# Performance work log

Measured on AMD Instinct MI355X. Metric: run time of the kernel, lower is better.

## Reference

```python
import jax, jax.numpy as jnp
import numpy as np

# Module constants (match init_kwargs)
E = 8           # num_experts
K = 2           # num_experts_per_tok
BLOCK = 16      # BLOCK_SIZE hardcoded in module
NORM_TOPK = True


def setup_inputs() -> dict:
    key = jax.random.key(0)
    k0, k1, k2, k3 = jax.random.split(key, 4)
    B, S, H = 2, 2048, 768
    F = 4 * H  # ffn_hidden_size
    x = jax.random.normal(k0, (B, S, H), dtype=jnp.float32)
    router_w = jax.random.normal(k1, (E, H), dtype=jnp.float32) * 0.02
    # kaiming-uniform-ish scale for w1/w2
    w1 = jax.random.uniform(k2, (H, E * F), dtype=jnp.float32, minval=-1.0, maxval=1.0) * float(1.0 / np.sqrt(H))
    w2 = jax.random.uniform(k3, (E * F, H), dtype=jnp.float32, minval=-1.0, maxval=1.0) * float(1.0 / np.sqrt(E * F))
    return {"x": x, "router_w": router_w, "w1": w1, "w2": w2}


def _moe_forward(x, router_w, w1, w2):
    B, S, H = x.shape
    T = B * S
    x_flat = x.reshape(T, H)

    # Router
    router_logits = x_flat @ router_w.T                      # [T, E]
    rw = jax.nn.softmax(router_logits.astype(jnp.float32), axis=-1)
    top_w, sel = jax.lax.top_k(rw, K)                        # [T, K]
    if NORM_TOPK:
        top_w = top_w / top_w.sum(axis=-1, keepdims=True)
    top_w = top_w.astype(x.dtype)  # NOTE: computed but NOT applied in combine (faithful to source)

    # Block-padding multiplicities (faithful to source's duplicate-last-token padding bug):
    # assignments are sorted stably by expert; the LAST assignment of each expert's
    # group is duplicated pad_e = (-count_e) % BLOCK times and then scatter-added.
    sel_flat = sel.reshape(-1)                               # [T*K], token-major stable order
    flat_idx = jnp.arange(T * K, dtype=jnp.int32)
    counts = jax.ops.segment_sum(jnp.ones((T * K,), jnp.int32), sel_flat, num_segments=E)
    pad = (-counts) % BLOCK                                  # [E]
    last_idx = jax.ops.segment_max(flat_idx, sel_flat, num_segments=E)  # [E]
    mult = 1 + jnp.where(flat_idx == last_idx[sel_flat], pad[sel_flat], 0)  # [T*K]

    # Combine coefficients coef[t, e] = multiplicity of (token t, expert e) assignment
    token_ids = flat_idx // K
    coef = jnp.zeros((T, E), dtype=x.dtype).at[token_ids, sel_flat].add(mult.astype(x.dtype))

    # Expert FFNs: y1 = gelu(x @ W1_e) @ W2_e, combined with coef (NOT routing weights)
    F = w1.shape[1] // E
    w1e = w1.reshape(H, E, F)
    w2e = w2.reshape(E, F, H)
    out = jnp.zeros((T, H), dtype=x.dtype)
    for e in range(E):  # small fixed loop over experts
        h = jax.nn.gelu(x_flat @ w1e[:, e, :], approximate=False)  # [T, F]
        out = out + coef[:, e:e + 1] * (h @ w2e[e])                # [T, H]

    return out.reshape(B, S, H), router_logits


def reference(x, router_w, w1, w2):
    return _moe_forward(x, router_w, w1, w2)
```

## Files before the change

kernel.cpp:

```cpp
#include <hip/hip_runtime.h>
#include <math.h>

#define T_TOK 4096
#define H_DIM 768
#define E_NUM 8
#define F_DIM 3072
#define EF_DIM 24576
#define BK 64
#define SEG_MAX 9216
#define MAX_TILES 72

#define OFF_CNT      0
#define OFF_LAST     8
#define OFF_NT      40
#define OFF_TOTAL   41
#define OFF_SCHED_E 48
#define OFF_SCHED_G 120

#define WS_SEL   768
#define WS_TOK   33536
#define WS_COEF  70400
#define WS_XG    107264ull
#define WS_HG    14263040ull
#define WS_WT    70886144ull

typedef __attribute__((ext_vector_type(8))) short short8;
typedef __attribute__((ext_vector_type(4))) float float4v;

__device__ __forceinline__ short f2b(float f) {
  union { float f; unsigned u; } v; v.f = f;
  unsigned r = v.u + 0x7FFFu + ((v.u >> 16) & 1u);
  return (short)(r >> 16);
}
__device__ __forceinline__ float gelu_fast(float v) {
  const float z = 1.5957691216f * fmaf(0.044715f * v * v, v, v);
  return v / (1.0f + __expf(-z));
}
__device__ __forceinline__ void gl_lds16(const void* g, void* l) {
  __builtin_amdgcn_global_load_lds(
      (const __attribute__((address_space(1))) void*)g,
      (__attribute__((address_space(3))) void*)l, 16, 0, 0);
}

__global__ __launch_bounds__(256) void router_k(const float* __restrict__ x,
                                                const float* __restrict__ rw,
                                                float* __restrict__ logits_out,
                                                int* __restrict__ sel) {
  __shared__ float rws[E_NUM * H_DIM];
  for (int i = threadIdx.x; i < E_NUM * H_DIM; i += 256) rws[i] = rw[i];
  __syncthreads();
  const int wid = threadIdx.x >> 6, lane = threadIdx.x & 63;
  const int t = blockIdx.x * 4 + wid;
  const float* xr = x + (size_t)t * H_DIM;
  double acc[E_NUM];
#pragma unroll
  for (int e = 0; e < E_NUM; ++e) acc[e] = 0.0;
  for (int i = 0; i < H_DIM / 64; ++i) {
    const int h = lane + 64 * i;
    const float xv = xr[h];
#pragma unroll
    for (int e = 0; e < E_NUM; ++e) acc[e] += (double)xv * (double)rws[e * H_DIM + h];
  }
#pragma unroll
  for (int e = 0; e < E_NUM; ++e)
    for (int off = 32; off; off >>= 1) acc[e] += __shfl_down(acc[e], off);
  if (lane == 0) {
    float lg[E_NUM];
#pragma unroll
    for (int e = 0; e < E_NUM; ++e) { lg[e] = (float)acc[e]; logits_out[t * E_NUM + e] = lg[e]; }
    int e0 = 0;
    for (int e = 1; e < E_NUM; ++e) if (lg[e] > lg[e0]) e0 = e;
    int e1 = -1;
    for (int e = 0; e < E_NUM; ++e) {
      if (e == e0) continue;
      if (e1 < 0 || lg[e] > lg[e1]) e1 = e;
    }
    sel[t * 2 + 0] = e0;
    sel[t * 2 + 1] = e1;
  }
}

__global__ __launch_bounds__(1024) void hist_k(const int* __restrict__ sel,
                                               int* __restrict__ meta) {
  const int e = blockIdx.x;
  const int tid = threadIdx.x, lane = tid & 63, wid = tid >> 6;
  __shared__ int wcnt[16], wlast[16];
  int c = 0, lmax = 0;
#pragma unroll
  for (int it = 0; it < 8; ++it) {
    const int a = it * 1024 + tid;
    const unsigned long long mask = __ballot(sel[a] == e);
    if (lane == 0 && mask) {
      c += (int)__popcll(mask);
      const int hi = 63 - (int)__clzll((long long)mask);
      const int cand = a + hi + 1;
      lmax = lmax > cand ? lmax : cand;
    }
  }
  if (lane == 0) { wcnt[wid] = c; wlast[wid] = lmax; }
  __syncthreads();
  if (tid == 0) {
    int C = 0, L = 0;
    for (int w = 0; w < 16; ++w) { C += wcnt[w]; L = L > wlast[w] ? L : wlast[w]; }
    meta[OFF_CNT + e] = C;
    meta[OFF_LAST + e] = L;
  }
}

__global__ __launch_bounds__(1024) void scatter_k(const int* __restrict__ sel,
                                                  int* __restrict__ meta,
                                                  int* __restrict__ tok,
                                                  float* __restrict__ coefv) {
  const int e = blockIdx.x;
  const int tid = threadIdx.x, lane = tid & 63, wid = tid >> 6;
  __shared__ int wv[16];

  int cnt[E_NUM];
#pragma unroll
  for (int i = 0; i < E_NUM; ++i) cnt[i] = meta[OFF_CNT + i];
  int seg = 0;
  for (int i = 0; i < e; ++i) seg += (cnt[i] + 127) & ~127;
  const int c = cnt[e];
  const int ru = (c + 127) & ~127;
  const int pad = (16 - (c & 15)) & 15;
  const int laste = meta[OFF_LAST + e];
  const float lastcoef = (float)(1 + pad);

  for (int p = c + tid; p < ru; p += 1024) { tok[seg + p] = -1; coefv[seg + p] = 0.0f; }
  if (e == E_NUM - 1) {
    const int total = seg + ru;
    for (int p = total + tid; p < SEG_MAX; p += 1024) { tok[p] = -1; coefv[p] = 0.0f; }
  }

  if (e == 0) {
    int nt = 0, s2 = 0;
    for (int i = 0; i < E_NUM; ++i) {
      const int rui = (cnt[i] + 127) & ~127;
      for (int m = 0; m < rui; m += 128) {
        if (nt == tid) { meta[OFF_SCHED_E + nt] = i; meta[OFF_SCHED_G + nt] = s2 + m; }
        ++nt;
      }
      s2 += rui;
    }
    if (tid >= nt && tid < MAX_TILES) { meta[OFF_SCHED_E + tid] = -1; meta[OFF_SCHED_G + tid] = 0; }
    if (tid == 0) { meta[OFF_NT] = nt; meta[OFF_TOTAL] = s2; }
  }

  int running = 0;
#pragma unroll
  for (int it = 0; it < 8; ++it) {
    const int a = it * 1024 + tid;
    const bool f = (sel[a] == e);
    const unsigned long long mask = __ballot(f);
    if (lane == 0) wv[wid] = (int)__popcll(mask);
    __syncthreads();
    int pre = 0, tot = 0;
#pragma unroll
    for (int w = 0; w < 16; ++w) { const int v = wv[w]; pre += (w < wid) ? v : 0; tot += v; }
    if (f) {
      const int rank = (int)__popcll(mask & ((1ull << lane) - 1ull));
      const int g = seg + running + pre + rank;
      tok[g] = a >> 1;
      coefv[g] = (laste == a + 1) ? lastcoef : 1.0f;
    }
    running += tot;
    __syncthreads();
  }
}

__global__ __launch_bounds__(256) void gather_x_k(const float* __restrict__ x,
                                                  const int* __restrict__ tok,
                                                  short* __restrict__ xg) {
  const int u = blockIdx.x * 256 + threadIdx.x;
  const int g = u / 96;
  const int c = (u - g * 96) * 8;
  const int t = tok[g];
  short8 v = {0, 0, 0, 0, 0, 0, 0, 0};
  if (t >= 0) {
    const float* src = x + (size_t)t * H_DIM + c;
    float4v f0 = *(const float4v*)src;
    float4v f1 = *(const float4v*)(src + 4);
    v[0] = f2b(f0[0]); v[1] = f2b(f0[1]); v[2] = f2b(f0[2]); v[3] = f2b(f0[3]);
    v[4] = f2b(f1[0]); v[5] = f2b(f1[1]); v[6] = f2b(f1[2]); v[7] = f2b(f1[3]);
  }
  *(short8*)&xg[(size_t)g * H_DIM + c] = v;
}

__global__ __launch_bounds__(256) void conv_w1_k(const float* __restrict__ w1, short* __restrict__ w1t) {
  __shared__ float tile[64][65];
  const int n0 = blockIdx.x * 64;
  const int h0 = blockIdx.y * 64;
  const int tid = threadIdx.x;
  const int rr = tid >> 4;
  const int cc = (tid & 15) * 4;
#pragma unroll
  for (int p = 0; p < 4; ++p) {
    const int r = p * 16 + rr;
    float4v f = *(const float4v*)(w1 + (size_t)(h0 + r) * EF_DIM + n0 + cc);
    tile[r][cc] = f[0]; tile[r][cc + 1] = f[1]; tile[r][cc + 2] = f[2]; tile[r][cc + 3] = f[3];
  }
  __syncthreads();
#pragma unroll
  for (int p = 0; p < 2; ++p) {
    const int item = p * 256 + tid;
    const int nl = item >> 3;
    const int u8 = (item & 7) * 8;
    short8 v;
#pragma unroll
    for (int j = 0; j < 8; ++j) v[j] = f2b(tile[u8 + j][nl]);
    *(short8*)(w1t + (size_t)(n0 + nl) * H_DIM + h0 + u8) = v;
  }
}

__global__ __launch_bounds__(256) void conv_w2_k(const float* __restrict__ w2, short* __restrict__ w2t) {
  __shared__ float tile[64][65];
  const int k0 = blockIdx.x * 64;
  const int h0 = blockIdx.y * 64;
  const int e = k0 / F_DIM;
  const int f0 = k0 - e * F_DIM;
  const int tid = threadIdx.x;
  const int rr = tid >> 4;
  const int cc = (tid & 15) * 4;
#pragma unroll
  for (int p = 0; p < 4; ++p) {
    const int r = p * 16 + rr;
    float4v f = *(const float4v*)(w2 + (size_t)(k0 + r) * H_DIM + h0 + cc);
    tile[r][cc] = f[0]; tile[r][cc + 1] = f[1]; tile[r][cc + 2] = f[2]; tile[r][cc + 3] = f[3];
  }
  __syncthreads();
#pragma unroll
  for (int p = 0; p < 2; ++p) {
    const int item = p * 256 + tid;
    const int nl = item >> 3;
    const int u8 = (item & 7) * 8;
    short8 v;
#pragma unroll
    for (int j = 0; j < 8; ++j) v[j] = f2b(tile[u8 + j][nl]);
    *(short8*)(w2t + (size_t)(e * H_DIM + h0 + nl) * F_DIM + f0 + u8) = v;
  }
}


__global__ __launch_bounds__(256) void gemm1_k(const short* __restrict__ xg,
                                               const short* __restrict__ w1t,
                                               const int* __restrict__ meta,
                                               short* __restrict__ hg) {
  const unsigned hwL = blockIdx.x;
  const unsigned logical = (hwL & 7u) * 216u + (hwL >> 3);
  const int slot = (int)(logical / 24u);
  const int n0 = (int)(logical % 24u) * 128;
  if (slot >= meta[OFF_NT]) return;
  const int e = meta[OFF_SCHED_E + slot];
  const int gbase = meta[OFF_SCHED_G + slot];

  __shared__ short As[128 * BK];
  __shared__ short Bs[128 * BK];

  const int tid = threadIdx.x;
  const int w = tid >> 6, l = tid & 63;
  const int mw = (w & 1) * 64, nw = (w >> 1) * 64;
  const int lrow = l & 15, q = l >> 4;

  const int srow = l >> 3;
  const int schunk = (l & 7) ^ srow;
  const short* agp[4];
  const short* bgp[4];
  short* alp[4];
  short* blp[4];
#pragma unroll
  for (int i = 0; i < 4; ++i) {
    const int r = i * 32 + w * 8 + srow;
    agp[i] = xg + (size_t)(gbase + r) * H_DIM + schunk * 8;
    bgp[i] = w1t + (size_t)(e * F_DIM + n0 + r) * H_DIM + schunk * 8;
    alp[i] = &As[(i * 32 + w * 8) * BK + l * 8];
    blp[i] = &Bs[(i * 32 + w * 8) * BK + l * 8];
  }
  const int rsw = lrow & 7;

  float4v acc[4][4] = {};

  for (int k0 = 0; k0 < H_DIM; k0 += BK) {
#pragma unroll
    for (int i = 0; i < 4; ++i) gl_lds16(agp[i] + k0, alp[i]);
#pragma unroll
    for (int i = 0; i < 4; ++i) gl_lds16(bgp[i] + k0, blp[i]);
    __syncthreads();
#pragma unroll
    for (int s = 0; s < 2; ++s) {
      short8 a_frag[4], b_frag[4];
      const int csw = ((s * 4 + q) ^ rsw) * 8;
#pragma unroll
      for (int i = 0; i < 4; ++i) a_frag[i] = *(const short8*)&As[(mw + 16 * i + lrow) * BK + csw];
#pragma unroll
      for (int j = 0; j < 4; ++j) b_frag[j] = *(const short8*)&Bs[(nw + 16 * j + lrow) * BK + csw];
#pragma unroll
      for (int i = 0; i < 4; ++i)
#pragma unroll
        for (int j = 0; j < 4; ++j)
          acc[i][j] = __builtin_amdgcn_mfma_f32_16x16x32_bf16(a_frag[i], b_frag[j], acc[i][j], 0, 0, 0);
    }
    __syncthreads();
  }
#pragma unroll
  for (int i = 0; i < 4; ++i)
#pragma unroll
    for (int j = 0; j < 4; ++j)
#pragma unroll
      for (int r = 0; r < 4; ++r) {
        const int row = mw + 16 * i + q * 4 + r;
        const int col = nw + 16 * j + lrow;
        hg[(size_t)(gbase + row) * F_DIM + n0 + col] = f2b(gelu_fast(acc[i][j][r]));
      }
}

__global__ __launch_bounds__(256) void gemm2_k(const short* __restrict__ hg,
                                               const short* __restrict__ w2t,
                                               const int* __restrict__ meta,
                                               const int* __restrict__ tok,
                                               const float* __restrict__ coefv,
                                               float* __restrict__ out) {
  const unsigned hwL = blockIdx.x;
  const unsigned logical = (hwL & 7u) * 108u + (hwL >> 3);
  const int slot = (int)(logical / 12u);
  const unsigned rem = logical % 12u;
  const int kz = (int)(rem / 6u);
  const int n0 = (int)(rem % 6u) * 128;
  if (slot >= meta[OFF_NT]) return;
  const int e = meta[OFF_SCHED_E + slot];
  const int gbase = meta[OFF_SCHED_G + slot];
  const int kbase = kz * (F_DIM / 2);

  __shared__ short As[128 * BK];
  __shared__ short Bs[128 * BK];

  const int tid = threadIdx.x;
  const int w = tid >> 6, l = tid & 63;
  const int mw = (w & 1) * 64, nw = (w >> 1) * 64;
  const int lrow = l & 15, q = l >> 4;

  const int srow = l >> 3;
  const int schunk = (l & 7) ^ srow;
  const short* agp[4];
  const short* bgp[4];
  short* alp[4];
  short* blp[4];
#pragma unroll
  for (int i = 0; i < 4; ++i) {
    const int r = i * 32 + w * 8 + srow;
    agp[i] = hg + (size_t)(gbase + r) * F_DIM + kbase + schunk * 8;
    bgp[i] = w2t + (size_t)(e * H_DIM + n0 + r) * F_DIM + kbase + schunk * 8;
    alp[i] = &As[(i * 32 + w * 8) * BK + l * 8];
    blp[i] = &Bs[(i * 32 + w * 8) * BK + l * 8];
  }
  const int rsw = lrow & 7;

  float4v acc[4][4] = {};

  for (int k0 = 0; k0 < F_DIM / 2; k0 += BK) {
#pragma unroll
    for (int i = 0; i < 4; ++i) gl_lds16(agp[i] + k0, alp[i]);
#pragma unroll
    for (int i = 0; i < 4; ++i) gl_lds16(bgp[i] + k0, blp[i]);
    __syncthreads();
#pragma unroll
    for (int s = 0; s < 2; ++s) {
      short8 a_frag[4], b_frag[4];
      const int csw = ((s * 4 + q) ^ rsw) * 8;
#pragma unroll
      for (int i = 0; i < 4; ++i) a_frag[i] = *(const short8*)&As[(mw + 16 * i + lrow) * BK + csw];
#pragma unroll
      for (int j = 0; j < 4; ++j) b_frag[j] = *(const short8*)&Bs[(nw + 16 * j + lrow) * BK + csw];
#pragma unroll
      for (int i = 0; i < 4; ++i)
#pragma unroll
        for (int j = 0; j < 4; ++j)
          acc[i][j] = __builtin_amdgcn_mfma_f32_16x16x32_bf16(a_frag[i], b_frag[j], acc[i][j], 0, 0, 0);
    }
    __syncthreads();
  }
#pragma unroll
  for (int i = 0; i < 4; ++i)
#pragma unroll
    for (int r = 0; r < 4; ++r) {
      const int row = mw + 16 * i + q * 4 + r;
      const int g = gbase + row;
      const int t = tok[g];
      if (t < 0) continue;
      const float cf = coefv[g];
#pragma unroll
      for (int j = 0; j < 4; ++j) {
        const int col = nw + 16 * j + lrow;
        atomicAdd(&out[(size_t)t * H_DIM + n0 + col], cf * acc[i][j][r]);
      }
    }
}

extern "C" void kernel_launch(void* const* d_in, const int* in_sizes, int n_in,
                              void* d_out, int out_size, void* d_ws, size_t ws_size,
                              hipStream_t stream) {
  const float* x  = (const float*)d_in[0];
  const float* rw = (const float*)d_in[1];
  const float* w1 = (const float*)d_in[2];
  const float* w2 = (const float*)d_in[3];
  float* out = (float*)d_out;
  float* logits = out + (size_t)T_TOK * H_DIM;

  char* ws = (char*)d_ws;
  int*   meta  = (int*)ws;
  int*   sel   = (int*)(ws + WS_SEL);
  int*   tok   = (int*)(ws + WS_TOK);
  float* coefv = (float*)(ws + WS_COEF);
  short* xg    = (short*)(ws + WS_XG);
  short* hg    = (short*)(ws + WS_HG);
  short* wt    = (short*)(ws + WS_WT);

  hipMemsetAsync(d_out, 0, (size_t)T_TOK * H_DIM * sizeof(float), stream);

  conv_w1_k<<<dim3(EF_DIM / 64, H_DIM / 64), 256, 0, stream>>>(w1, wt);
  router_k<<<T_TOK / 4, 256, 0, stream>>>(x, rw, logits, sel);
  hist_k<<<E_NUM, 1024, 0, stream>>>(sel, meta);
  scatter_k<<<E_NUM, 1024, 0, stream>>>(sel, meta, tok, coefv);
  gather_x_k<<<(SEG_MAX * (H_DIM / 8)) / 256, 256, 0, stream>>>(x, tok, xg);
  gemm1_k<<<24 * MAX_TILES, 256, 0, stream>>>(xg, wt, meta, hg);
  conv_w2_k<<<dim3(EF_DIM / 64, H_DIM / 64), 256, 0, stream>>>(w2, wt);
  gemm2_k<<<6 * MAX_TILES * 2, 256, 0, stream>>>(hg, wt, meta, tok, coefv, out);
}
```

Before: 378.5 us.

## Double-buffer GEMM K-loops, stage epilogues via LDS, replace atomic combine with gather

Both expert GEMMs now double-buffer their LDS tiles so the next K slice is loaded while MFMAs run on the current one. Epilogues are staged through swizzled LDS so results go out as coalesced 16-byte stores. GEMM2 drops the split-K atomicAdd scatter and writes per-assignment bf16 partials. A new pos_k kernel inverts the permutation and a combine_k kernel sums each token's two expert outputs with their coefficients, which also removes the output memset. The cost is an extra bf16 rounding of the expert outputs, two extra launches, half as many GEMM2 blocks, and reuse of the sel and xg buffers for new data.

```diff
diff --git a/kernel.cpp b/kernel.cpp
--- a/kernel.cpp
+++ b/kernel.cpp
@@ -9,6 +9,7 @@
 #define BK 64
 #define SEG_MAX 9216
 #define MAX_TILES 72
+#define TILE_SH (128 * BK)
 
 #define OFF_CNT      0
 #define OFF_LAST     8
@@ -31,6 +32,10 @@
   union { float f; unsigned u; } v; v.f = f;
   unsigned r = v.u + 0x7FFFu + ((v.u >> 16) & 1u);
   return (short)(r >> 16);
+}
+__device__ __forceinline__ float b2f(short s) {
+  union { unsigned u; float f; } v; v.u = ((unsigned)(unsigned short)s) << 16;
+  return v.f;
 }
 __device__ __forceinline__ float gelu_fast(float v) {
   const float z = 1.5957691216f * fmaf(0.044715f * v * v, v, v);
@@ -160,12 +165,18 @@
     if (f) {
       const int rank = (int)__popcll(mask & ((1ull << lane) - 1ull));
       const int g = seg + running + pre + rank;
-      tok[g] = a >> 1;
+      tok[g] = a;
       coefv[g] = (laste == a + 1) ? lastcoef : 1.0f;
     }
     running += tot;
     __syncthreads();
   }
+}
+
+__global__ __launch_bounds__(256) void pos_k(const int* __restrict__ tok, int* __restrict__ pos) {
+  const int g = blockIdx.x * 256 + threadIdx.x;
+  const int a = tok[g];
+  if (a >= 0) pos[a] = g;
 }
 
 __global__ __launch_bounds__(256) void gather_x_k(const float* __restrict__ x,
@@ -174,10 +185,10 @@
   const int u = blockIdx.x * 256 + threadIdx.x;
   const int g = u / 96;
   const int c = (u - g * 96) * 8;
-  const int t = tok[g];
+  const int a = tok[g];
   short8 v = {0, 0, 0, 0, 0, 0, 0, 0};
-  if (t >= 0) {
-    const float* src = x + (size_t)t * H_DIM + c;
+  if (a >= 0) {
+    const float* src = x + (size_t)(a >> 1) * H_DIM + c;
     float4v f0 = *(const float4v*)src;
     float4v f1 = *(const float4v*)(src + 4);
     v[0] = f2b(f0[0]); v[1] = f2b(f0[1]); v[2] = f2b(f0[2]); v[3] = f2b(f0[3]);
@@ -253,54 +264,67 @@
   const int e = meta[OFF_SCHED_E + slot];
   const int gbase = meta[OFF_SCHED_G + slot];
 
-  __shared__ short As[128 * BK];
-  __shared__ short Bs[128 * BK];
+  __shared__ short As[2 * TILE_SH];
+  __shared__ short Bs[2 * TILE_SH];
 
   const int tid = threadIdx.x;
   const int w = tid >> 6, l = tid & 63;
   const int mw = (w & 1) * 64, nw = (w >> 1) * 64;
   const int lrow = l & 15, q = l >> 4;
-
   const int srow = l >> 3;
   const int schunk = (l & 7) ^ srow;
+
   const short* agp[4];
   const short* bgp[4];
-  short* alp[4];
-  short* blp[4];
+  int loff[4];
 #pragma unroll
   for (int i = 0; i < 4; ++i) {
     const int r = i * 32 + w * 8 + srow;
     agp[i] = xg + (size_t)(gbase + r) * H_DIM + schunk * 8;
     bgp[i] = w1t + (size_t)(e * F_DIM + n0 + r) * H_DIM + schunk * 8;
-    alp[i] = &As[(i * 32 + w * 8) * BK + l * 8];
-    blp[i] = &Bs[(i * 32 + w * 8) * BK + l * 8];
+    loff[i] = (i * 32 + w * 8) * BK + l * 8;
   }
   const int rsw = lrow & 7;
 
   float4v acc[4][4] = {};
 
-  for (int k0 = 0; k0 < H_DIM; k0 += BK) {
-#pragma unroll
-    for (int i = 0; i < 4; ++i) gl_lds16(agp[i] + k0, alp[i]);
-#pragma unroll
-    for (int i = 0; i < 4; ++i) gl_lds16(bgp[i] + k0, blp[i]);
-    __syncthreads();
+#pragma unroll
+  for (int i = 0; i < 4; ++i) gl_lds16(agp[i], &As[loff[i]]);
+#pragma unroll
+  for (int i = 0; i < 4; ++i) gl_lds16(bgp[i], &Bs[loff[i]]);
+  asm volatile("s_waitcnt vmcnt(0)" ::: "memory");
+  __builtin_amdgcn_s_barrier();
+
+  const int NT = H_DIM / BK;
+  for (int t = 0; t < NT; ++t) {
+    const int cb = (t & 1) * TILE_SH;
+    const int nb = TILE_SH - cb;
+    if (t + 1 < NT) {
+      const int k0 = (t + 1) * BK;
+#pragma unroll
+      for (int i = 0; i < 4; ++i) gl_lds16(agp[i] + k0, &As[nb + loff[i]]);
+#pragma unroll
+      for (int i = 0; i < 4; ++i) gl_lds16(bgp[i] + k0, &Bs[nb + loff[i]]);
+    }
 #pragma unroll
     for (int s = 0; s < 2; ++s) {
       short8 a_frag[4], b_frag[4];
       const int csw = ((s * 4 + q) ^ rsw) * 8;
 #pragma unroll
-      for (int i = 0; i < 4; ++i) a_frag[i] = *(const short8*)&As[(mw + 16 * i + lrow) * BK + csw];
-#pragma unroll
-      for (int j = 0; j < 4; ++j) b_frag[j] = *(const short8*)&Bs[(nw + 16 * j + lrow) * BK + csw];
+      for (int i = 0; i < 4; ++i) a_frag[i] = *(const short8*)&As[cb + (mw + 16 * i + lrow) * BK + csw];
+#pragma unroll
+      for (int j = 0; j < 4; ++j) b_frag[j] = *(const short8*)&Bs[cb + (nw + 16 * j + lrow) * BK + csw];
 #pragma unroll
       for (int i = 0; i < 4; ++i)
 #pragma unroll
         for (int j = 0; j < 4; ++j)
           acc[i][j] = __builtin_amdgcn_mfma_f32_16x16x32_bf16(a_frag[i], b_frag[j], acc[i][j], 0, 0, 0);
     }
-    __syncthreads();
-  }
+    asm volatile("s_waitcnt vmcnt(0) lgkmcnt(0)" ::: "memory");
+    __builtin_amdgcn_s_barrier();
+  }
+
+  short* Ep = As;
 #pragma unroll
   for (int i = 0; i < 4; ++i)
 #pragma unroll
@@ -309,90 +333,132 @@
       for (int r = 0; r < 4; ++r) {
         const int row = mw + 16 * i + q * 4 + r;
         const int col = nw + 16 * j + lrow;
-        hg[(size_t)(gbase + row) * F_DIM + n0 + col] = f2b(gelu_fast(acc[i][j][r]));
+        Ep[row * 128 + (col ^ ((row & 7) << 4))] = f2b(gelu_fast(acc[i][j][r]));
       }
+  __syncthreads();
+#pragma unroll
+  for (int p = 0; p < 8; ++p) {
+    const int item = p * 256 + tid;
+    const int row = item >> 4;
+    const int cc8 = (item & 15) * 8;
+    const short8 v = *(const short8*)&Ep[row * 128 + (cc8 ^ ((row & 7) << 4))];
+    *(short8*)&hg[(size_t)(gbase + row) * F_DIM + n0 + cc8] = v;
+  }
 }
 
 __global__ __launch_bounds__(256) void gemm2_k(const short* __restrict__ hg,
                                                const short* __restrict__ w2t,
                                                const int* __restrict__ meta,
-                                               const int* __restrict__ tok,
-                                               const float* __restrict__ coefv,
-                                               float* __restrict__ out) {
+                                               short* __restrict__ tmp) {
   const unsigned hwL = blockIdx.x;
-  const unsigned logical = (hwL & 7u) * 108u + (hwL >> 3);
-  const int slot = (int)(logical / 12u);
-  const unsigned rem = logical % 12u;
-  const int kz = (int)(rem / 6u);
-  const int n0 = (int)(rem % 6u) * 128;
+  const unsigned logical = (hwL & 7u) * 54u + (hwL >> 3);
+  const int slot = (int)(logical / 6u);
+  const int n0 = (int)(logical % 6u) * 128;
   if (slot >= meta[OFF_NT]) return;
   const int e = meta[OFF_SCHED_E + slot];
   const int gbase = meta[OFF_SCHED_G + slot];
-  const int kbase = kz * (F_DIM / 2);
-
-  __shared__ short As[128 * BK];
-  __shared__ short Bs[128 * BK];
+
+  __shared__ short As[2 * TILE_SH];
+  __shared__ short Bs[2 * TILE_SH];
 
   const int tid = threadIdx.x;
   const int w = tid >> 6, l = tid & 63;
   const int mw = (w & 1) * 64, nw = (w >> 1) * 64;
   const int lrow = l & 15, q = l >> 4;
-
   const int srow = l >> 3;
   const int schunk = (l & 7) ^ srow;
+
   const short* agp[4];
   const short* bgp[4];
-  short* alp[4];
-  short* blp[4];
+  int loff[4];
 #pragma unroll
   for (int i = 0; i < 4; ++i) {
     const int r = i * 32 + w * 8 + srow;
-    agp[i] = hg + (size_t)(gbase + r) * F_DIM + kbase + schunk * 8;
-    bgp[i] = w2t + (size_t)(e * H_DIM + n0 + r) * F_DIM + kbase + schunk * 8;
-    alp[i] = &As[(i * 32 + w * 8) * BK + l * 8];
-    blp[i] = &Bs[(i * 32 + w * 8) * BK + l * 8];
+    agp[i] = hg + (size_t)(gbase + r) * F_DIM + schunk * 8;
+    bgp[i] = w2t + (size_t)(e * H_DIM + n0 + r) * F_DIM + schunk * 8;
+    loff[i] = (i * 32 + w * 8) * BK + l * 8;
   }
   const int rsw = lrow & 7;
 
   float4v acc[4][4] = {};
 
-  for (int k0 = 0; k0 < F_DIM / 2; k0 += BK) {
-#pragma unroll
-    for (int i = 0; i < 4; ++i) gl_lds16(agp[i] + k0, alp[i]);
-#pragma unroll
-    for (int i = 0; i < 4; ++i) gl_lds16(bgp[i] + k0, blp[i]);
-    __syncthreads();
+#pragma unroll
+  for (int i = 0; i < 4; ++i) gl_lds16(agp[i], &As[loff[i]]);
+#pragma unroll
+  for (int i = 0; i < 4; ++i) gl_lds16(bgp[i], &Bs[loff[i]]);
+  asm volatile("s_waitcnt vmcnt(0)" ::: "memory");
+  __builtin_amdgcn_s_barrier();
+
+  const int NT = F_DIM / BK;
+  for (int t = 0; t < NT; ++t) {
+    const int cb = (t & 1) * TILE_SH;
+    const int nb = TILE_SH - cb;
+    if (t + 1 < NT) {
+      const int k0 = (t + 1) * BK;
+#pragma unroll
+      for (int i = 0; i < 4; ++i) gl_lds16(agp[i] + k0, &As[nb + loff[i]]);
+#pragma unroll
+      for (int i = 0; i < 4; ++i) gl_lds16(bgp[i] + k0, &Bs[nb + loff[i]]);
+    }
 #pragma unroll
     for (int s = 0; s < 2; ++s) {
       short8 a_frag[4], b_frag[4];
       const int csw = ((s * 4 + q) ^ rsw) * 8;
 #pragma unroll
-      for (int i = 0; i < 4; ++i) a_frag[i] = *(const short8*)&As[(mw + 16 * i + lrow) * BK + csw];
-#pragma unroll
-      for (int j = 0; j < 4; ++j) b_frag[j] = *(const short8*)&Bs[(nw + 16 * j + lrow) * BK + csw];
+      for (int i = 0; i < 4; ++i) a_frag[i] = *(const short8*)&As[cb + (mw + 16 * i + lrow) * BK + csw];
+#pragma unroll
+      for (int j = 0; j < 4; ++j) b_frag[j] = *(const short8*)&Bs[cb + (nw + 16 * j + lrow) * BK + csw];
 #pragma unroll
       for (int i = 0; i < 4; ++i)
 #pragma unroll
         for (int j = 0; j < 4; ++j)
           acc[i][j] = __builtin_amdgcn_mfma_f32_16x16x32_bf16(a_frag[i], b_frag[j], acc[i][j], 0, 0, 0);
     }
-    __syncthreads();
-  }
+    asm volatile("s_waitcnt vmcnt(0) lgkmcnt(0)" ::: "memory");
+    __builtin_amdgcn_s_barrier();
+  }
+
+  short* Ep = As;
 #pragma unroll
   for (int i = 0; i < 4; ++i)
 #pragma unroll
-    for (int r = 0; r < 4; ++r) {
-      const int row = mw + 16 * i + q * 4 + r;
-      const int g = gbase + row;
-      const int t = tok[g];
-      if (t < 0) continue;
-      const float cf = coefv[g];
-#pragma unroll
-      for (int j = 0; j < 4; ++j) {
+    for (int j = 0; j < 4; ++j)
+#pragma unroll
+      for (int r = 0; r < 4; ++r) {
+        const int row = mw + 16 * i + q * 4 + r;
         const int col = nw + 16 * j + lrow;
-        atomicAdd(&out[(size_t)t * H_DIM + n0 + col], cf * acc[i][j][r]);
+        Ep[row * 128 + (col ^ ((row & 7) << 4))] = f2b(acc[i][j][r]);
       }
-    }
+  __syncthreads();
+#pragma unroll
+  for (int p = 0; p < 8; ++p) {
+    const int item = p * 256 + tid;
+    const int row = item >> 4;
+    const int cc8 = (item & 15) * 8;
+    const short8 v = *(const short8*)&Ep[row * 128 + (cc8 ^ ((row & 7) << 4))];
+    *(short8*)&tmp[(size_t)(gbase + row) * H_DIM + n0 + cc8] = v;
+  }
+}
+
+__global__ __launch_bounds__(256) void combine_k(const short* __restrict__ tmp,
+                                                 const int* __restrict__ pos,
+                                                 const float* __restrict__ coefv,
+                                                 float* __restrict__ out) {
+  const int u = blockIdx.x * 256 + threadIdx.x;
+  const int t = u / 96;
+  const int c = (u - t * 96) * 8;
+  const int g0 = pos[t * 2 + 0];
+  const int g1 = pos[t * 2 + 1];
+  const float c0 = coefv[g0];
+  const float c1 = coefv[g1];
+  const short8 v0 = *(const short8*)&tmp[(size_t)g0 * H_DIM + c];
+  const short8 v1 = *(const short8*)&tmp[(size_t)g1 * H_DIM + c];
+  float r[8];
+#pragma unroll
+  for (int j = 0; j < 8; ++j) r[j] = c0 * b2f(v0[j]) + c1 * b2f(v1[j]);
+  float4v* dst = (float4v*)&out[(size_t)t * H_DIM + c];
+  dst[0] = (float4v){r[0], r[1], r[2], r[3]};
+  dst[1] = (float4v){r[4], r[5], r[6], r[7]};
 }
 
 extern "C" void kernel_launch(void* const* d_in, const int* in_sizes, int n_in,
@@ -414,14 +480,14 @@
   short* hg    = (short*)(ws + WS_HG);
   short* wt    = (short*)(ws + WS_WT);
 
-  hipMemsetAsync(d_out, 0, (size_t)T_TOK * H_DIM * sizeof(float), stream);
-
   conv_w1_k<<<dim3(EF_DIM / 64, H_DIM / 64), 256, 0, stream>>>(w1, wt);
   router_k<<<T_TOK / 4, 256, 0, stream>>>(x, rw, logits, sel);
   hist_k<<<E_NUM, 1024, 0, stream>>>(sel, meta);
   scatter_k<<<E_NUM, 1024, 0, stream>>>(sel, meta, tok, coefv);
+  pos_k<<<SEG_MAX / 256, 256, 0, stream>>>(tok, sel);
   gather_x_k<<<(SEG_MAX * (H_DIM / 8)) / 256, 256, 0, stream>>>(x, tok, xg);
   gemm1_k<<<24 * MAX_TILES, 256, 0, stream>>>(xg, wt, meta, hg);
   conv_w2_k<<<dim3(EF_DIM / 64, H_DIM / 64), 256, 0, stream>>>(w2, wt);
-  gemm2_k<<<6 * MAX_TILES * 2, 256, 0, stream>>>(hg, wt, meta, tok, coefv, out);
-}
+  gemm2_k<<<6 * MAX_TILES, 256, 0, stream>>>(hg, wt, meta, xg);
+  combine_k<<<(T_TOK * 96) / 256, 256, 0, stream>>>(xg, sel, coefv, out);
+}
```

Result: faster. 358.6 us (-5.2%).
